# Optimization experiments

Hardware: AMD Instinct MI355X
Metric: run time of the kernel (lower is better)

Reference implementation:

```python
import jax, jax.numpy as jnp
import numpy as np

B, N, IN_DIM, OUT_DIM, H = 8, 1024, 256, 256, 4
HD = OUT_DIM // H  # head_dim = 64
NEG = -1e9
EPS = 1e-5


def setup_inputs() -> dict:
    key = jax.random.key(0)
    ks = jax.random.split(key, 9)
    h = jax.random.normal(ks[0], (B, N, IN_DIM), dtype=jnp.float32)
    adj = jax.random.randint(ks[1], (N, N), 0, 2, dtype=jnp.int32)
    adj = adj.at[jnp.arange(N), jnp.arange(N)].set(1)  # self loops so no empty rows
    s = 1.0 / np.sqrt(IN_DIM)
    W = jax.random.uniform(ks[2], (H, IN_DIM, HD), jnp.float32, -s, s)
    sa = 1.0 / np.sqrt(2 * HD)
    a1 = jax.random.uniform(ks[3], (H, HD), jnp.float32, -sa, sa)
    a2 = jax.random.uniform(ks[4], (H, HD), jnp.float32, -sa, sa)
    sp = 1.0 / np.sqrt(OUT_DIM)
    proj_w = jax.random.uniform(ks[5], (OUT_DIM, OUT_DIM), jnp.float32, -sp, sp)
    proj_b = jax.random.uniform(ks[6], (OUT_DIM,), jnp.float32, -sp, sp)
    gamma = jnp.ones((OUT_DIM,), jnp.float32)
    beta = jnp.zeros((OUT_DIM,), jnp.float32)
    return {"h": h, "adj": adj, "W": W, "a1": a1, "a2": a2,
            "proj_w": proj_w, "proj_b": proj_b, "gamma": gamma, "beta": beta}


def reference(h, adj, W, a1, a2, proj_w, proj_b, gamma, beta):
    # Wh: [B,H,N,HD]
    Wh = jnp.einsum('bni,hid->bhnd', h, W)
    # Decompose a([Wh_i || Wh_j]) = a1.Wh_i + a2.Wh_j (same math as concat+linear)
    si = jnp.einsum('bhnd,hd->bhn', Wh, a1)  # [B,H,N]
    sj = jnp.einsum('bhnd,hd->bhn', Wh, a2)
    e = jax.nn.leaky_relu(si[:, :, :, None] + sj[:, :, None, :], 0.2)  # [B,H,N,N]
    mask = (adj == 0)  # [N,N]
    e = jnp.where(mask[None, None], NEG, e)
    alpha = jax.nn.softmax(e, axis=-1)
    out = jnp.einsum('bhnm,bhmd->bhnd', alpha, Wh)  # [B,H,N,HD]
    h_multi = out.transpose(0, 2, 1, 3).reshape(B, N, OUT_DIM)  # concat heads
    h_out = jnp.einsum('bnd,od->bno', h_multi, proj_w) + proj_b
    h_out = h_out + h  # residual (in_dim == out_dim)
    mu = jnp.mean(h_out, axis=-1, keepdims=True)
    var = jnp.mean(jnp.square(h_out - mu), axis=-1, keepdims=True)
    return (h_out - mu) * jax.lax.rsqrt(var + EPS) * gamma + beta
```

## Files before the change

kernel.cpp:

```cpp
#include <hip/hip_runtime.h>
#include <hip/hip_bf16.h>

#define NN 1024

typedef __attribute__((ext_vector_type(8))) short short8;
typedef __attribute__((ext_vector_type(4))) short short4e;
typedef __attribute__((ext_vector_type(4))) float floatx4;
typedef __attribute__((ext_vector_type(4))) int intx4;

static __device__ __forceinline__ short bfb(float x) {
    return (short)__bfloat16_as_ushort(__float2bfloat16(x));
}

__global__ __launch_bounds__(256) void wh_kernel(
    const float* __restrict__ h, const float* __restrict__ W,
    const float* __restrict__ a1, const float* __restrict__ a2,
    const float* __restrict__ proj_w, const int* __restrict__ adj,
    __hip_bfloat16* __restrict__ WhT,
    float* __restrict__ si, float* __restrict__ sj,
    __hip_bfloat16* __restrict__ pwb,
    unsigned* __restrict__ adjm)
{
    int blk = blockIdx.x, t = threadIdx.x;

    if (blk >= 512) {
        if (blk < 528) {
            size_t base = (size_t)(blk - 512) * 4096 + (size_t)t * 16;
            #pragma unroll
            for (int k = 0; k < 16; k += 4) {
                floatx4 v = *(const floatx4*)(proj_w + base + k);
                alignas(8) __hip_bfloat16 tmp[4];
                #pragma unroll
                for (int j = 0; j < 4; ++j) tmp[j] = __float2bfloat16(v[j]);
                *(short4e*)(pwb + base + k) = *(const short4e*)tmp;
            }
        } else {
            int n = (blk - 528) * 8 + (t >> 5);
            int wd = t & 31;
            const int* arow = adj + (size_t)n * NN + wd * 32;
            unsigned bits = 0;
            #pragma unroll
            for (int j4 = 0; j4 < 8; ++j4) {
                intx4 v = *(const intx4*)(arow + j4 * 4);
                #pragma unroll
                for (int j = 0; j < 4; ++j) if (v[j] != 0) bits |= (1u << (j4 * 4 + j));
            }
            adjm[(size_t)n * 32 + wd] = bits;
        }
        return;
    }

    int w = t >> 6, l = t & 63;
    int rl = l & 15, q = l >> 4;
    int r0 = blk * 16;
    int bb = r0 >> 10;
    int n0 = r0 & 1023;

    __shared__ float redsi[4][4][16];
    __shared__ float redsj[4][4][16];

    short8 af[8];
    const float* Arow = h + (size_t)(r0 + rl) * 256 + q * 8;
    #pragma unroll
    for (int k0 = 0; k0 < 8; ++k0) {
        floatx4 v0 = *(const floatx4*)(Arow + k0 * 32);
        floatx4 v1 = *(const floatx4*)(Arow + k0 * 32 + 4);
        short8 a;
        #pragma unroll
        for (int j = 0; j < 4; ++j) { a[j] = bfb(v0[j]); a[j + 4] = bfb(v1[j]); }
        af[k0] = a;
    }

    float a1v[4], a2v[4];
    #pragma unroll
    for (int j = 0; j < 4; ++j) {
        a1v[j] = a1[j * 64 + w * 16 + rl];
        a2v[j] = a2[j * 64 + w * 16 + rl];
    }

    #pragma unroll
    for (int j = 0; j < 4; ++j) {
        int ct = w + j * 4;
        const float* Wb = W + (size_t)(ct >> 2) * 16384 + (ct & 3) * 16 + rl;
        floatx4 acc = {0.f, 0.f, 0.f, 0.f};
        #pragma unroll
        for (int k0 = 0; k0 < 8; ++k0) {
            short8 bfr;
            #pragma unroll
            for (int jj = 0; jj < 8; ++jj)
                bfr[jj] = bfb(Wb[(size_t)(k0 * 32 + q * 8 + jj) * 64]);
            acc = __builtin_amdgcn_mfma_f32_16x16x32_bf16(af[k0], bfr, acc, 0, 0, 0);
        }

        alignas(8) __hip_bfloat16 tmp[4];
        #pragma unroll
        for (int i = 0; i < 4; ++i) tmp[i] = __float2bfloat16(acc[i]);
        *(short4e*)(WhT + ((size_t)(bb * 4 + j) * 64 + w * 16 + rl) * NN + n0 + q * 4) =
            *(const short4e*)tmp;

        #pragma unroll
        for (int i = 0; i < 4; ++i) {
            float p1 = acc[i] * a1v[j];
            float p2 = acc[i] * a2v[j];
            #pragma unroll
            for (int off = 1; off < 16; off <<= 1) {
                p1 += __shfl_xor(p1, off, 64);
                p2 += __shfl_xor(p2, off, 64);
            }
            if (rl == 0) { redsi[w][j][q * 4 + i] = p1; redsj[w][j][q * 4 + i] = p2; }
        }
    }
    __syncthreads();

    if (w == 0) {
        int head = l >> 4, row = l & 15;
        float s = redsi[0][head][row] + redsi[1][head][row] + redsi[2][head][row] + redsi[3][head][row];
        si[(size_t)(bb * 4 + head) * NN + n0 + row] = s;
    } else if (w == 1) {
        int head = l >> 4, row = l & 15;
        float s = redsj[0][head][row] + redsj[1][head][row] + redsj[2][head][row] + redsj[3][head][row];
        sj[(size_t)(bb * 4 + head) * NN + n0 + row] = s;
    }
}

__global__ __launch_bounds__(256) void attn_proj_kernel(
    const unsigned* __restrict__ adjm,
    const __hip_bfloat16* __restrict__ WhT,
    const float* __restrict__ si, const float* __restrict__ sj,
    const __hip_bfloat16* __restrict__ pwb,
    const float* __restrict__ h,
    const float* __restrict__ proj_b, const float* __restrict__ gamma,
    const float* __restrict__ beta,
    float* __restrict__ out)
{
    int blk = blockIdx.x, t = threadIdx.x;
    int w = t >> 6, l = t & 63;
    int rl = l & 15, q = l >> 4;
    int b = blk >> 6, n0 = (blk & 63) * 16;
    int bh = b * 4 + w;
    int r0 = blk * 16;

    __shared__ __align__(16) __hip_bfloat16 p_lds[4][16 * 136];
    __shared__ __align__(16) __hip_bfloat16 hm_stage[16][264];
    __shared__ float rinvs[4][16];
    __shared__ float red[2][4][16];

    int r = l >> 2, cg = l & 3;
    float sii = si[(size_t)bh * NN + n0 + r];
    const float* sjr = sj + (size_t)bh * NN;
    const unsigned* amrow = adjm + (size_t)(n0 + r) * 32;

    __hip_bfloat16* pt = &p_lds[w][0];
    const __hip_bfloat16* Ab = pt + rl * 136 + q * 8;
    const __hip_bfloat16* Bbase = WhT + ((size_t)bh * 64 + rl) * NN + q * 8;

    float lsum = 0.f;
    floatx4 acc[4] = { {0,0,0,0}, {0,0,0,0}, {0,0,0,0}, {0,0,0,0} };

    for (int m0 = 0; m0 < NN; m0 += 128) {
        int mb = m0 + cg * 32;
        unsigned bits = amrow[mb >> 5];
        alignas(16) __hip_bfloat16 tmp[32];
        #pragma unroll
        for (int c4 = 0; c4 < 8; ++c4) {
            floatx4 s4 = *(const floatx4*)(sjr + mb + c4 * 4);
            #pragma unroll
            for (int k = 0; k < 4; ++k) {
                float x = sii + s4[k];
                x = x > 0.f ? x : 0.2f * x;
                x = ((bits >> (c4 * 4 + k)) & 1u) ? x : -1e9f;
                float pv = __expf(x);
                lsum += pv;
                tmp[c4 * 4 + k] = __float2bfloat16(pv);
            }
        }
        {
            short8* dst = (short8*)(pt + r * 136 + cg * 32);
            const short8* srcv = (const short8*)tmp;
            dst[0] = srcv[0]; dst[1] = srcv[1]; dst[2] = srcv[2]; dst[3] = srcv[3];
        }
        #pragma unroll
        for (int ks = 0; ks < 4; ++ks) {
            short8 afr = *(const short8*)(Ab + ks * 32);
            #pragma unroll
            for (int dt = 0; dt < 4; ++dt) {
                short8 bfr = *(const short8*)(Bbase + (size_t)dt * 16 * NN + m0 + ks * 32);
                acc[dt] = __builtin_amdgcn_mfma_f32_16x16x32_bf16(afr, bfr, acc[dt], 0, 0, 0);
            }
        }
    }

    lsum += __shfl_xor(lsum, 1, 64);
    lsum += __shfl_xor(lsum, 2, 64);
    if (cg == 0) rinvs[w][r] = 1.f / lsum;
    float riv[4];
    #pragma unroll
    for (int i = 0; i < 4; ++i) riv[i] = rinvs[w][q * 4 + i];

    #pragma unroll
    for (int dt = 0; dt < 4; ++dt) {
        #pragma unroll
        for (int i = 0; i < 4; ++i)
            hm_stage[q * 4 + i][w * 64 + dt * 16 + rl] = __float2bfloat16(acc[dt][i] * riv[i]);
    }
    __syncthreads();

    short8 paf[8];
    const __hip_bfloat16* Arow2 = &hm_stage[rl][0] + q * 8;
    #pragma unroll
    for (int k0 = 0; k0 < 8; ++k0) paf[k0] = *(const short8*)(Arow2 + k0 * 32);

    floatx4 pacc[4];
    #pragma unroll
    for (int j = 0; j < 4; ++j) {
        int ct = w + j * 4;
        const __hip_bfloat16* Brow = pwb + (size_t)(ct * 16 + rl) * 256 + q * 8;
        floatx4 a = {0.f, 0.f, 0.f, 0.f};
        #pragma unroll
        for (int k0 = 0; k0 < 8; ++k0) {
            short8 bfr = *(const short8*)(Brow + k0 * 32);
            a = __builtin_amdgcn_mfma_f32_16x16x32_bf16(paf[k0], bfr, a, 0, 0, 0);
        }
        pacc[j] = a;
    }

    float ps[4] = {0.f, 0.f, 0.f, 0.f};
    #pragma unroll
    for (int j = 0; j < 4; ++j) {
        int col = (w + j * 4) * 16 + rl;
        float pb = proj_b[col];
        #pragma unroll
        for (int i = 0; i < 4; ++i) {
            float v = pacc[j][i] + pb + h[(size_t)(r0 + q * 4 + i) * 256 + col];
            pacc[j][i] = v;
            ps[i] += v;
        }
    }
    #pragma unroll
    for (int i = 0; i < 4; ++i) {
        float s = ps[i];
        #pragma unroll
        for (int off = 1; off < 16; off <<= 1) s += __shfl_xor(s, off, 64);
        ps[i] = s;
    }
    if (rl == 0) {
        for (int i = 0; i < 4; ++i) red[0][w][q * 4 + i] = ps[i];
    }
    __syncthreads();
    float mu[4];
    #pragma unroll
    for (int i = 0; i < 4; ++i) {
        int row = q * 4 + i;
        mu[i] = (red[0][0][row] + red[0][1][row] + red[0][2][row] + red[0][3][row]) * (1.f / 256.f);
    }

    float vs[4] = {0.f, 0.f, 0.f, 0.f};
    #pragma unroll
    for (int j = 0; j < 4; ++j) {
        #pragma unroll
        for (int i = 0; i < 4; ++i) { float cv = pacc[j][i] - mu[i]; vs[i] += cv * cv; }
    }
    #pragma unroll
    for (int i = 0; i < 4; ++i) {
        float s = vs[i];
        #pragma unroll
        for (int off = 1; off < 16; off <<= 1) s += __shfl_xor(s, off, 64);
        vs[i] = s;
    }
    if (rl == 0) {
        for (int i = 0; i < 4; ++i) red[1][w][q * 4 + i] = vs[i];
    }
    __syncthreads();
    float rs[4];
    #pragma unroll
    for (int i = 0; i < 4; ++i) {
        int row = q * 4 + i;
        float var = (red[1][0][row] + red[1][1][row] + red[1][2][row] + red[1][3][row]) * (1.f / 256.f);
        rs[i] = rsqrtf(var + 1e-5f);
    }
    #pragma unroll
    for (int j = 0; j < 4; ++j) {
        int col = (w + j * 4) * 16 + rl;
        float g = gamma[col], be = beta[col];
        #pragma unroll
        for (int i = 0; i < 4; ++i)
            out[(size_t)(r0 + q * 4 + i) * 256 + col] = (pacc[j][i] - mu[i]) * rs[i] * g + be;
    }
}

extern "C" void kernel_launch(void* const* d_in, const int* in_sizes, int n_in,
                              void* d_out, int out_size, void* d_ws, size_t ws_size,
                              hipStream_t stream) {
    const float* h      = (const float*)d_in[0];
    const int*   adj    = (const int*)d_in[1];
    const float* W      = (const float*)d_in[2];
    const float* a1     = (const float*)d_in[3];
    const float* a2     = (const float*)d_in[4];
    const float* proj_w = (const float*)d_in[5];
    const float* proj_b = (const float*)d_in[6];
    const float* gamma  = (const float*)d_in[7];
    const float* beta   = (const float*)d_in[8];
    float* out = (float*)d_out;

    char* ws = (char*)d_ws;
    __hip_bfloat16* WhT = (__hip_bfloat16*)ws;   ws += (size_t)32 * 64 * NN * 2;
    __hip_bfloat16* pwb = (__hip_bfloat16*)ws;   ws += 256 * 256 * 2;
    float* si = (float*)ws;                      ws += (size_t)32 * NN * 4;
    float* sj = (float*)ws;                      ws += (size_t)32 * NN * 4;
    unsigned* adjm = (unsigned*)ws;              ws += (size_t)NN * 32 * 4;

    wh_kernel<<<656, 256, 0, stream>>>(h, W, a1, a2, proj_w, adj, WhT, si, sj, pwb, adjm);
    attn_proj_kernel<<<512, 256, 0, stream>>>(adjm, WhT, si, sj, pwb, h, proj_b, gamma, beta, out);
}
```

Before: 147.4 us.

## Pre-transpose W to bf16 and software-pipeline B-operand loads in GEMM loops

Adds a prep kernel that converts W into a transposed bf16 layout (along with the existing proj_w conversion and adjacency bitmask packing). This lets wh_kernel load B fragments as contiguous 16-byte vectors instead of strided scalar fp32 loads with per-element conversion, and it prefetches the next head's fragments in registers. In attn_proj_kernel the main loop is fully unrolled so the next tile of WhT fragments is loaded and the next score block computed while the current tile's MFMAs run. The cost is one extra kernel launch and serialization, plus higher register pressure that may reduce occupancy.

```diff
diff --git a/kernel.cpp b/kernel.cpp
--- a/kernel.cpp
+++ b/kernel.cpp
@@ -12,47 +12,58 @@
     return (short)__bfloat16_as_ushort(__float2bfloat16(x));
 }
 
-__global__ __launch_bounds__(256) void wh_kernel(
-    const float* __restrict__ h, const float* __restrict__ W,
-    const float* __restrict__ a1, const float* __restrict__ a2,
-    const float* __restrict__ proj_w, const int* __restrict__ adj,
-    __hip_bfloat16* __restrict__ WhT,
-    float* __restrict__ si, float* __restrict__ sj,
+__global__ __launch_bounds__(256) void prep_kernel(
+    const float* __restrict__ W, const float* __restrict__ proj_w,
+    const int* __restrict__ adj,
+    __hip_bfloat16* __restrict__ WTb,
     __hip_bfloat16* __restrict__ pwb,
     unsigned* __restrict__ adjm)
 {
     int blk = blockIdx.x, t = threadIdx.x;
-
-    if (blk >= 512) {
-        if (blk < 528) {
-            size_t base = (size_t)(blk - 512) * 4096 + (size_t)t * 16;
-            #pragma unroll
-            for (int k = 0; k < 16; k += 4) {
-                floatx4 v = *(const floatx4*)(proj_w + base + k);
-                alignas(8) __hip_bfloat16 tmp[4];
-                #pragma unroll
-                for (int j = 0; j < 4; ++j) tmp[j] = __float2bfloat16(v[j]);
-                *(short4e*)(pwb + base + k) = *(const short4e*)tmp;
-            }
-        } else {
-            int n = (blk - 528) * 8 + (t >> 5);
-            int wd = t & 31;
-            const int* arow = adj + (size_t)n * NN + wd * 32;
-            unsigned bits = 0;
-            #pragma unroll
-            for (int j4 = 0; j4 < 8; ++j4) {
-                intx4 v = *(const intx4*)(arow + j4 * 4);
-                #pragma unroll
-                for (int j = 0; j < 4; ++j) if (v[j] != 0) bits |= (1u << (j4 * 4 + j));
-            }
-            adjm[(size_t)n * 32 + wd] = bits;
-        }
-        return;
-    }
-
+    if (blk < 16) {
+        int o = blk * 16 + (t >> 4);
+        int hh = o >> 6, d = o & 63;
+        #pragma unroll
+        for (int kk = 0; kk < 16; ++kk) {
+            int k = (t & 15) + 16 * kk;
+            WTb[(size_t)o * 256 + k] = __float2bfloat16(W[((size_t)hh * 256 + k) * 64 + d]);
+        }
+    } else if (blk < 32) {
+        size_t base = (size_t)(blk - 16) * 4096 + (size_t)t * 16;
+        #pragma unroll
+        for (int k = 0; k < 16; k += 4) {
+            floatx4 v = *(const floatx4*)(proj_w + base + k);
+            short4e tmp;
+            #pragma unroll
+            for (int j = 0; j < 4; ++j) tmp[j] = bfb(v[j]);
+            *(short4e*)(pwb + base + k) = tmp;
+        }
+    } else {
+        int n = (blk - 32) * 8 + (t >> 5);
+        int wd = t & 31;
+        const int* arow = adj + (size_t)n * NN + wd * 32;
+        unsigned bits = 0;
+        #pragma unroll
+        for (int j4 = 0; j4 < 8; ++j4) {
+            intx4 v = *(const intx4*)(arow + j4 * 4);
+            #pragma unroll
+            for (int j = 0; j < 4; ++j) if (v[j] != 0) bits |= (1u << (j4 * 4 + j));
+        }
+        adjm[(size_t)n * 32 + wd] = bits;
+    }
+}
+
+__global__ __launch_bounds__(256) void wh_kernel(
+    const float* __restrict__ h,
+    const __hip_bfloat16* __restrict__ WTb,
+    const float* __restrict__ a1, const float* __restrict__ a2,
+    __hip_bfloat16* __restrict__ WhT,
+    float* __restrict__ si, float* __restrict__ sj)
+{
+    int t = threadIdx.x;
     int w = t >> 6, l = t & 63;
     int rl = l & 15, q = l >> 4;
-    int r0 = blk * 16;
+    int r0 = blockIdx.x * 16;
     int bb = r0 >> 10;
     int n0 = r0 & 1023;
 
@@ -78,25 +89,31 @@
         a2v[j] = a2[j * 64 + w * 16 + rl];
     }
 
-    #pragma unroll
-    for (int j = 0; j < 4; ++j) {
-        int ct = w + j * 4;
-        const float* Wb = W + (size_t)(ct >> 2) * 16384 + (ct & 3) * 16 + rl;
+    short8 bcur[8];
+    {
+        const __hip_bfloat16* B0 = WTb + (size_t)(w * 16 + rl) * 256 + q * 8;
+        #pragma unroll
+        for (int k0 = 0; k0 < 8; ++k0) bcur[k0] = *(const short8*)(B0 + k0 * 32);
+    }
+
+    #pragma unroll
+    for (int j = 0; j < 4; ++j) {
+        short8 bnxt[8];
+        if (j < 3) {
+            const __hip_bfloat16* Bn = WTb + (size_t)((w + (j + 1) * 4) * 16 + rl) * 256 + q * 8;
+            #pragma unroll
+            for (int k0 = 0; k0 < 8; ++k0) bnxt[k0] = *(const short8*)(Bn + k0 * 32);
+        }
+
         floatx4 acc = {0.f, 0.f, 0.f, 0.f};
         #pragma unroll
-        for (int k0 = 0; k0 < 8; ++k0) {
-            short8 bfr;
-            #pragma unroll
-            for (int jj = 0; jj < 8; ++jj)
-                bfr[jj] = bfb(Wb[(size_t)(k0 * 32 + q * 8 + jj) * 64]);
-            acc = __builtin_amdgcn_mfma_f32_16x16x32_bf16(af[k0], bfr, acc, 0, 0, 0);
-        }
-
-        alignas(8) __hip_bfloat16 tmp[4];
-        #pragma unroll
-        for (int i = 0; i < 4; ++i) tmp[i] = __float2bfloat16(acc[i]);
-        *(short4e*)(WhT + ((size_t)(bb * 4 + j) * 64 + w * 16 + rl) * NN + n0 + q * 4) =
-            *(const short4e*)tmp;
+        for (int k0 = 0; k0 < 8; ++k0)
+            acc = __builtin_amdgcn_mfma_f32_16x16x32_bf16(af[k0], bcur[k0], acc, 0, 0, 0);
+
+        short4e tmp;
+        #pragma unroll
+        for (int i = 0; i < 4; ++i) tmp[i] = bfb(acc[i]);
+        *(short4e*)(WhT + ((size_t)(bb * 4 + j) * 64 + w * 16 + rl) * NN + n0 + q * 4) = tmp;
 
         #pragma unroll
         for (int i = 0; i < 4; ++i) {
@@ -109,6 +126,9 @@
             }
             if (rl == 0) { redsi[w][j][q * 4 + i] = p1; redsj[w][j][q * 4 + i] = p2; }
         }
+
+        #pragma unroll
+        for (int z = 0; z < 8; ++z) bcur[z] = bnxt[z];
     }
     __syncthreads();
 
@@ -157,38 +177,61 @@
     float lsum = 0.f;
     floatx4 acc[4] = { {0,0,0,0}, {0,0,0,0}, {0,0,0,0}, {0,0,0,0} };
 
-    for (int m0 = 0; m0 < NN; m0 += 128) {
-        int mb = m0 + cg * 32;
-        unsigned bits = amrow[mb >> 5];
-        alignas(16) __hip_bfloat16 tmp[32];
-        #pragma unroll
-        for (int c4 = 0; c4 < 8; ++c4) {
-            floatx4 s4 = *(const floatx4*)(sjr + mb + c4 * 4);
-            #pragma unroll
-            for (int k = 0; k < 4; ++k) {
-                float x = sii + s4[k];
-                x = x > 0.f ? x : 0.2f * x;
-                x = ((bits >> (c4 * 4 + k)) & 1u) ? x : -1e9f;
-                float pv = __expf(x);
-                lsum += pv;
-                tmp[c4 * 4 + k] = __float2bfloat16(pv);
-            }
-        }
-        {
-            short8* dst = (short8*)(pt + r * 136 + cg * 32);
-            const short8* srcv = (const short8*)tmp;
-            dst[0] = srcv[0]; dst[1] = srcv[1]; dst[2] = srcv[2]; dst[3] = srcv[3];
+#define SCORE_BLOCK(ITX)                                                        \
+    do {                                                                        \
+        int mb_ = (ITX) * 128 + cg * 32;                                        \
+        unsigned bits_ = amrow[mb_ >> 5];                                       \
+        short8 pv_[4];                                                          \
+        _Pragma("unroll")                                                       \
+        for (int c4 = 0; c4 < 8; ++c4) {                                        \
+            floatx4 s4_ = *(const floatx4*)(sjr + mb_ + c4 * 4);                \
+            _Pragma("unroll")                                                   \
+            for (int k = 0; k < 4; ++k) {                                       \
+                float x_ = sii + s4_[k];                                        \
+                x_ = x_ > 0.f ? x_ : 0.2f * x_;                                 \
+                x_ = ((bits_ >> (c4 * 4 + k)) & 1u) ? x_ : -1e9f;               \
+                float pv = __expf(x_);                                          \
+                lsum += pv;                                                     \
+                pv_[c4 >> 1][(c4 & 1) * 4 + k] = bfb(pv);                       \
+            }                                                                   \
+        }                                                                       \
+        short8* dst_ = (short8*)(pt + r * 136 + cg * 32);                       \
+        dst_[0] = pv_[0]; dst_[1] = pv_[1]; dst_[2] = pv_[2]; dst_[3] = pv_[3]; \
+    } while (0)
+
+    short8 bcur[16];
+    #pragma unroll
+    for (int ks = 0; ks < 4; ++ks)
+        #pragma unroll
+        for (int dt = 0; dt < 4; ++dt)
+            bcur[ks * 4 + dt] = *(const short8*)(Bbase + (size_t)dt * 16 * NN + ks * 32);
+    SCORE_BLOCK(0);
+
+    #pragma unroll
+    for (int it = 0; it < 8; ++it) {
+        short8 bnxt[16];
+        if (it < 7) {
+            int m1 = (it + 1) * 128;
+            #pragma unroll
+            for (int ks = 0; ks < 4; ++ks)
+                #pragma unroll
+                for (int dt = 0; dt < 4; ++dt)
+                    bnxt[ks * 4 + dt] = *(const short8*)(Bbase + (size_t)dt * 16 * NN + m1 + ks * 32);
         }
         #pragma unroll
         for (int ks = 0; ks < 4; ++ks) {
             short8 afr = *(const short8*)(Ab + ks * 32);
             #pragma unroll
-            for (int dt = 0; dt < 4; ++dt) {
-                short8 bfr = *(const short8*)(Bbase + (size_t)dt * 16 * NN + m0 + ks * 32);
-                acc[dt] = __builtin_amdgcn_mfma_f32_16x16x32_bf16(afr, bfr, acc[dt], 0, 0, 0);
-            }
-        }
-    }
+            for (int dt = 0; dt < 4; ++dt)
+                acc[dt] = __builtin_amdgcn_mfma_f32_16x16x32_bf16(afr, bcur[ks * 4 + dt], acc[dt], 0, 0, 0);
+        }
+        if (it < 7) {
+            SCORE_BLOCK(it + 1);
+            #pragma unroll
+            for (int z = 0; z < 16; ++z) bcur[z] = bnxt[z];
+        }
+    }
+#undef SCORE_BLOCK
 
     lsum += __shfl_xor(lsum, 1, 64);
     lsum += __shfl_xor(lsum, 2, 64);
@@ -304,11 +347,13 @@
 
     char* ws = (char*)d_ws;
     __hip_bfloat16* WhT = (__hip_bfloat16*)ws;   ws += (size_t)32 * 64 * NN * 2;
+    __hip_bfloat16* WTb = (__hip_bfloat16*)ws;   ws += 256 * 256 * 2;
     __hip_bfloat16* pwb = (__hip_bfloat16*)ws;   ws += 256 * 256 * 2;
     float* si = (float*)ws;                      ws += (size_t)32 * NN * 4;
     float* sj = (float*)ws;                      ws += (size_t)32 * NN * 4;
     unsigned* adjm = (unsigned*)ws;              ws += (size_t)NN * 32 * 4;
 
-    wh_kernel<<<656, 256, 0, stream>>>(h, W, a1, a2, proj_w, adj, WhT, si, sj, pwb, adjm);
+    prep_kernel<<<160, 256, 0, stream>>>(W, proj_w, adj, WTb, pwb, adjm);
+    wh_kernel<<<512, 256, 0, stream>>>(h, WTb, a1, a2, WhT, si, sj);
     attn_proj_kernel<<<512, 256, 0, stream>>>(adjm, WhT, si, sj, pwb, h, proj_b, gamma, beta, out);
 }
```

Measured after the change: 146.0 us. About the same (-1.0%).

## Double block size to 512 threads and split attention key range across wave pairs

Applied to the files above, without the earlier changes.

Both kernels move to 512-thread blocks. In the attention kernel each head now gets two waves, and each wave processes half of the key dimension. The partial softmax sums and partial outputs are combined through LDS in fp32 before the projection, and each wave computes half as many projection column tiles. The aim is more waves in flight per block and a shorter serial loop over keys on a grid of only 512 blocks, at the cost of extra LDS traffic, an extra barrier and higher LDS usage per block.

```diff
diff --git a/kernel.cpp b/kernel.cpp
--- a/kernel.cpp
+++ b/kernel.cpp
@@ -12,7 +12,7 @@
     return (short)__bfloat16_as_ushort(__float2bfloat16(x));
 }
 
-__global__ __launch_bounds__(256) void wh_kernel(
+__global__ __launch_bounds__(512, 4) void wh_kernel(
     const float* __restrict__ h, const float* __restrict__ W,
     const float* __restrict__ a1, const float* __restrict__ a2,
     const float* __restrict__ proj_w, const int* __restrict__ adj,
@@ -24,19 +24,19 @@
     int blk = blockIdx.x, t = threadIdx.x;
 
     if (blk >= 512) {
-        if (blk < 528) {
-            size_t base = (size_t)(blk - 512) * 4096 + (size_t)t * 16;
+        if (blk < 520) {
+            size_t base = (size_t)(blk - 512) * 8192 + (size_t)t * 16;
             #pragma unroll
             for (int k = 0; k < 16; k += 4) {
                 floatx4 v = *(const floatx4*)(proj_w + base + k);
-                alignas(8) __hip_bfloat16 tmp[4];
+                short4e tmp;
                 #pragma unroll
-                for (int j = 0; j < 4; ++j) tmp[j] = __float2bfloat16(v[j]);
-                *(short4e*)(pwb + base + k) = *(const short4e*)tmp;
+                for (int j = 0; j < 4; ++j) tmp[j] = bfb(v[j]);
+                *(short4e*)(pwb + base + k) = tmp;
             }
         } else {
-            int n = (blk - 528) * 8 + (t >> 5);
-            int wd = t & 31;
+            int idx = (blk - 520) * 512 + t;
+            int n = idx >> 5, wd = idx & 31;
             const int* arow = adj + (size_t)n * NN + wd * 32;
             unsigned bits = 0;
             #pragma unroll
@@ -56,8 +56,8 @@
     int bb = r0 >> 10;
     int n0 = r0 & 1023;
 
-    __shared__ float redsi[4][4][16];
-    __shared__ float redsj[4][4][16];
+    __shared__ float redsi[16][16];
+    __shared__ float redsj[16][16];
 
     short8 af[8];
     const float* Arow = h + (size_t)(r0 + rl) * 256 + q * 8;
@@ -71,17 +71,12 @@
         af[k0] = a;
     }
 
-    float a1v[4], a2v[4];
-    #pragma unroll
-    for (int j = 0; j < 4; ++j) {
-        a1v[j] = a1[j * 64 + w * 16 + rl];
-        a2v[j] = a2[j * 64 + w * 16 + rl];
-    }
-
-    #pragma unroll
-    for (int j = 0; j < 4; ++j) {
-        int ct = w + j * 4;
-        const float* Wb = W + (size_t)(ct >> 2) * 16384 + (ct & 3) * 16 + rl;
+    #pragma unroll
+    for (int j2 = 0; j2 < 2; ++j2) {
+        int ct = w + j2 * 8;
+        int hh = ct >> 2, ds = ct & 3;
+        const float* Wb = W + (size_t)hh * 16384 + ds * 16 + rl;
+
         floatx4 acc = {0.f, 0.f, 0.f, 0.f};
         #pragma unroll
         for (int k0 = 0; k0 < 8; ++k0) {
@@ -92,38 +87,42 @@
             acc = __builtin_amdgcn_mfma_f32_16x16x32_bf16(af[k0], bfr, acc, 0, 0, 0);
         }
 
-        alignas(8) __hip_bfloat16 tmp[4];
-        #pragma unroll
-        for (int i = 0; i < 4; ++i) tmp[i] = __float2bfloat16(acc[i]);
-        *(short4e*)(WhT + ((size_t)(bb * 4 + j) * 64 + w * 16 + rl) * NN + n0 + q * 4) =
-            *(const short4e*)tmp;
-
+        short4e tmp;
+        #pragma unroll
+        for (int i = 0; i < 4; ++i) tmp[i] = bfb(acc[i]);
+        *(short4e*)(WhT + ((size_t)(bb * 4 + hh) * 64 + ds * 16 + rl) * NN + n0 + q * 4) = tmp;
+
+        float av1 = a1[hh * 64 + ds * 16 + rl];
+        float av2 = a2[hh * 64 + ds * 16 + rl];
         #pragma unroll
         for (int i = 0; i < 4; ++i) {
-            float p1 = acc[i] * a1v[j];
-            float p2 = acc[i] * a2v[j];
+            float p1 = acc[i] * av1;
+            float p2 = acc[i] * av2;
             #pragma unroll
             for (int off = 1; off < 16; off <<= 1) {
                 p1 += __shfl_xor(p1, off, 64);
                 p2 += __shfl_xor(p2, off, 64);
             }
-            if (rl == 0) { redsi[w][j][q * 4 + i] = p1; redsj[w][j][q * 4 + i] = p2; }
-        }
-    }
-    __syncthreads();
-
-    if (w == 0) {
-        int head = l >> 4, row = l & 15;
-        float s = redsi[0][head][row] + redsi[1][head][row] + redsi[2][head][row] + redsi[3][head][row];
+            if (rl == 0) { redsi[ct][q * 4 + i] = p1; redsj[ct][q * 4 + i] = p2; }
+        }
+    }
+    __syncthreads();
+
+    if (t < 64) {
+        int head = t >> 4, row = t & 15;
+        float s = redsi[head * 4 + 0][row] + redsi[head * 4 + 1][row]
+                + redsi[head * 4 + 2][row] + redsi[head * 4 + 3][row];
         si[(size_t)(bb * 4 + head) * NN + n0 + row] = s;
-    } else if (w == 1) {
-        int head = l >> 4, row = l & 15;
-        float s = redsj[0][head][row] + redsj[1][head][row] + redsj[2][head][row] + redsj[3][head][row];
+    } else if (t < 128) {
+        int u = t - 64;
+        int head = u >> 4, row = u & 15;
+        float s = redsj[head * 4 + 0][row] + redsj[head * 4 + 1][row]
+                + redsj[head * 4 + 2][row] + redsj[head * 4 + 3][row];
         sj[(size_t)(bb * 4 + head) * NN + n0 + row] = s;
     }
 }
 
-__global__ __launch_bounds__(256) void attn_proj_kernel(
+__global__ __launch_bounds__(512, 4) void attn_proj_kernel(
     const unsigned* __restrict__ adjm,
     const __hip_bfloat16* __restrict__ WhT,
     const float* __restrict__ si, const float* __restrict__ sj,
@@ -136,14 +135,15 @@
     int blk = blockIdx.x, t = threadIdx.x;
     int w = t >> 6, l = t & 63;
     int rl = l & 15, q = l >> 4;
+    int head = w >> 1, half = w & 1;
     int b = blk >> 6, n0 = (blk & 63) * 16;
-    int bh = b * 4 + w;
+    int bh = b * 4 + head;
     int r0 = blk * 16;
 
-    __shared__ __align__(16) __hip_bfloat16 p_lds[4][16 * 136];
-    __shared__ __align__(16) __hip_bfloat16 hm_stage[16][264];
-    __shared__ float rinvs[4][16];
-    __shared__ float red[2][4][16];
+    __shared__ __align__(16) __hip_bfloat16 p_lds[8][16 * 136];
+    __shared__ float hmf[2][16][260];
+    __shared__ float lpart[4][2][16];
+    __shared__ float red[2][8][16];
 
     int r = l >> 2, cg = l & 3;
     float sii = si[(size_t)bh * NN + n0 + r];
@@ -157,10 +157,11 @@
     float lsum = 0.f;
     floatx4 acc[4] = { {0,0,0,0}, {0,0,0,0}, {0,0,0,0}, {0,0,0,0} };
 
-    for (int m0 = 0; m0 < NN; m0 += 128) {
+    for (int itt = 0; itt < 4; ++itt) {
+        int m0 = (half * 4 + itt) * 128;
         int mb = m0 + cg * 32;
         unsigned bits = amrow[mb >> 5];
-        alignas(16) __hip_bfloat16 tmp[32];
+        short8 pv_[4];
         #pragma unroll
         for (int c4 = 0; c4 < 8; ++c4) {
             floatx4 s4 = *(const floatx4*)(sjr + mb + c4 * 4);
@@ -171,13 +172,12 @@
                 x = ((bits >> (c4 * 4 + k)) & 1u) ? x : -1e9f;
                 float pv = __expf(x);
                 lsum += pv;
-                tmp[c4 * 4 + k] = __float2bfloat16(pv);
+                pv_[c4 >> 1][(c4 & 1) * 4 + k] = bfb(pv);
             }
         }
         {
             short8* dst = (short8*)(pt + r * 136 + cg * 32);
-            const short8* srcv = (const short8*)tmp;
-            dst[0] = srcv[0]; dst[1] = srcv[1]; dst[2] = srcv[2]; dst[3] = srcv[3];
+            dst[0] = pv_[0]; dst[1] = pv_[1]; dst[2] = pv_[2]; dst[3] = pv_[3];
         }
         #pragma unroll
         for (int ks = 0; ks < 4; ++ks) {
@@ -192,28 +192,40 @@
 
     lsum += __shfl_xor(lsum, 1, 64);
     lsum += __shfl_xor(lsum, 2, 64);
-    if (cg == 0) rinvs[w][r] = 1.f / lsum;
+    if (cg == 0) lpart[head][half][r] = lsum;
+    __syncthreads();
+
     float riv[4];
     #pragma unroll
-    for (int i = 0; i < 4; ++i) riv[i] = rinvs[w][q * 4 + i];
-
+    for (int i = 0; i < 4; ++i) {
+        int row = q * 4 + i;
+        riv[i] = 1.f / (lpart[head][0][row] + lpart[head][1][row]);
+    }
     #pragma unroll
     for (int dt = 0; dt < 4; ++dt) {
         #pragma unroll
         for (int i = 0; i < 4; ++i)
-            hm_stage[q * 4 + i][w * 64 + dt * 16 + rl] = __float2bfloat16(acc[dt][i] * riv[i]);
+            hmf[half][q * 4 + i][head * 64 + dt * 16 + rl] = acc[dt][i] * riv[i];
     }
     __syncthreads();
 
     short8 paf[8];
-    const __hip_bfloat16* Arow2 = &hm_stage[rl][0] + q * 8;
-    #pragma unroll
-    for (int k0 = 0; k0 < 8; ++k0) paf[k0] = *(const short8*)(Arow2 + k0 * 32);
-
-    floatx4 pacc[4];
-    #pragma unroll
-    for (int j = 0; j < 4; ++j) {
-        int ct = w + j * 4;
+    #pragma unroll
+    for (int k0 = 0; k0 < 8; ++k0) {
+        const float* h0 = &hmf[0][rl][k0 * 32 + q * 8];
+        const float* h1 = &hmf[1][rl][k0 * 32 + q * 8];
+        floatx4 a0 = *(const floatx4*)h0, a1v = *(const floatx4*)(h0 + 4);
+        floatx4 b0 = *(const floatx4*)h1, b1v = *(const floatx4*)(h1 + 4);
+        short8 a;
+        #pragma unroll
+        for (int j = 0; j < 4; ++j) { a[j] = bfb(a0[j] + b0[j]); a[j + 4] = bfb(a1v[j] + b1v[j]); }
+        paf[k0] = a;
+    }
+
+    floatx4 pacc[2];
+    #pragma unroll
+    for (int j2 = 0; j2 < 2; ++j2) {
+        int ct = w + j2 * 8;
         const __hip_bfloat16* Brow = pwb + (size_t)(ct * 16 + rl) * 256 + q * 8;
         floatx4 a = {0.f, 0.f, 0.f, 0.f};
         #pragma unroll
@@ -221,18 +233,18 @@
             short8 bfr = *(const short8*)(Brow + k0 * 32);
             a = __builtin_amdgcn_mfma_f32_16x16x32_bf16(paf[k0], bfr, a, 0, 0, 0);
         }
-        pacc[j] = a;
+        pacc[j2] = a;
     }
 
     float ps[4] = {0.f, 0.f, 0.f, 0.f};
     #pragma unroll
-    for (int j = 0; j < 4; ++j) {
-        int col = (w + j * 4) * 16 + rl;
+    for (int j2 = 0; j2 < 2; ++j2) {
+        int col = (w + j2 * 8) * 16 + rl;
         float pb = proj_b[col];
         #pragma unroll
         for (int i = 0; i < 4; ++i) {
-            float v = pacc[j][i] + pb + h[(size_t)(r0 + q * 4 + i) * 256 + col];
-            pacc[j][i] = v;
+            float v = pacc[j2][i] + pb + h[(size_t)(r0 + q * 4 + i) * 256 + col];
+            pacc[j2][i] = v;
             ps[i] += v;
         }
     }
@@ -251,14 +263,17 @@
     #pragma unroll
     for (int i = 0; i < 4; ++i) {
         int row = q * 4 + i;
-        mu[i] = (red[0][0][row] + red[0][1][row] + red[0][2][row] + red[0][3][row]) * (1.f / 256.f);
+        float s = 0.f;
+        #pragma unroll
+        for (int w2 = 0; w2 < 8; ++w2) s += red[0][w2][row];
+        mu[i] = s * (1.f / 256.f);
     }
 
     float vs[4] = {0.f, 0.f, 0.f, 0.f};
     #pragma unroll
-    for (int j = 0; j < 4; ++j) {
-        #pragma unroll
-        for (int i = 0; i < 4; ++i) { float cv = pacc[j][i] - mu[i]; vs[i] += cv * cv; }
+    for (int j2 = 0; j2 < 2; ++j2) {
+        #pragma unroll
+        for (int i = 0; i < 4; ++i) { float cv = pacc[j2][i] - mu[i]; vs[i] += cv * cv; }
     }
     #pragma unroll
     for (int i = 0; i < 4; ++i) {
@@ -275,16 +290,18 @@
     #pragma unroll
     for (int i = 0; i < 4; ++i) {
         int row = q * 4 + i;
-        float var = (red[1][0][row] + red[1][1][row] + red[1][2][row] + red[1][3][row]) * (1.f / 256.f);
-        rs[i] = rsqrtf(var + 1e-5f);
-    }
-    #pragma unroll
-    for (int j = 0; j < 4; ++j) {
-        int col = (w + j * 4) * 16 + rl;
+        float s = 0.f;
+        #pragma unroll
+        for (int w2 = 0; w2 < 8; ++w2) s += red[1][w2][row];
+        rs[i] = rsqrtf(s * (1.f / 256.f) + 1e-5f);
+    }
+    #pragma unroll
+    for (int j2 = 0; j2 < 2; ++j2) {
+        int col = (w + j2 * 8) * 16 + rl;
         float g = gamma[col], be = beta[col];
         #pragma unroll
         for (int i = 0; i < 4; ++i)
-            out[(size_t)(r0 + q * 4 + i) * 256 + col] = (pacc[j][i] - mu[i]) * rs[i] * g + be;
+            out[(size_t)(r0 + q * 4 + i) * 256 + col] = (pacc[j2][i] - mu[i]) * rs[i] * g + be;
     }
 }
 
@@ -309,6 +326,6 @@
     float* sj = (float*)ws;                      ws += (size_t)32 * NN * 4;
     unsigned* adjm = (unsigned*)ws;              ws += (size_t)NN * 32 * 4;
 
-    wh_kernel<<<656, 256, 0, stream>>>(h, W, a1, a2, proj_w, adj, WhT, si, sj, pwb, adjm);
-    attn_proj_kernel<<<512, 256, 0, stream>>>(adjm, WhT, si, sj, pwb, h, proj_b, gamma, beta, out);
+    wh_kernel<<<584, 512, 0, stream>>>(h, W, a1, a2, proj_w, adj, WhT, si, sj, pwb, adjm);
+    attn_proj_kernel<<<512, 512, 0, stream>>>(adjm, WhT, si, sj, pwb, h, proj_b, gamma, beta, out);
 }
```

Measured after the change: 169.3 us. 14.9% more time.
